# Optimization experiments

Measured on AMD Instinct MI355X. Metric: run time of the kernel, lower is better.

The kernel has to match this reference:

```python
import jax, jax.numpy as jnp
import numpy as np

REG_M = 0.1     # reg_m_bregman
N_ITER = 30     # fixed MM iteration count (POT uses numItermax=1000 w/ early stop)
EPS = 1e-16     # POT's stabilizer added to the denominator


def setup_inputs() -> dict:
    key = jax.random.key(0)
    kx, ky = jax.random.split(key)
    x = jax.random.normal(kx, (4096, 256), dtype=jnp.float32)
    y = jax.random.normal(ky, (4096, 256), dtype=jnp.float32)
    # L2-normalize embeddings so squared distances lie in [0,4] and the
    # KL kernel exp(-M / (2*reg_m)) stays in a representable range.
    x = x / jnp.linalg.norm(x, axis=1, keepdims=True)
    y = y / jnp.linalg.norm(y, axis=1, keepdims=True)
    return {"x": x, "y": y}


def reference(x, y):
    m, n = x.shape[0], y.shape[0]
    # ot.dist default metric: squared euclidean  M[i,j] = ||x_i - y_j||^2
    M = (jnp.sum(x * x, axis=1)[:, None]
         + jnp.sum(y * y, axis=1)[None, :]
         - 2.0 * (x @ y.T))                                  # [m, n]
    a = jnp.full((m,), 1.0 / m, dtype=x.dtype)
    b = jnp.full((n,), 1.0 / n, dtype=x.dtype)
    # POT mm_unbalanced, div='kl', reg_m1=reg_m2=reg_m, reg=0:
    # r1 = r2 = 1/2, K = sqrt(a_i b_j) * exp(-M / (2*reg_m)), G0 = a (x) b,
    # G <- K * G / (sqrt(rowsum_i) * sqrt(colsum_j) + eps)
    K = jnp.sqrt(a[:, None] * b[None, :]) * jnp.exp(-M / (2.0 * REG_M))
    G0 = a[:, None] * b[None, :]

    def step(G, _):
        Gd = jnp.sqrt(G.sum(axis=1)[:, None] * G.sum(axis=0)[None, :]) + EPS
        return K * G / Gd, None

    Pi, _ = jax.lax.scan(step, G0, None, length=N_ITER)
    # (Pi @ M.T).mean() = sum_j (sum_i Pi[i,j]) * (sum_k M[k,j]) / m^2
    return jnp.dot(Pi.sum(axis=0), M.sum(axis=0)) / (m * m)
```

## Files before the change

### kernel.cpp

```cpp
#include <hip/hip_runtime.h>
#include <math.h>

#define MDIM 4096
#define NDIM 4096
#define DDIM 256
#define N_ITER 30

#define TWO_KAPPA 14.426950408889634
#define CLCONST  (-12.0 - TWO_KAPPA)

typedef __attribute__((ext_vector_type(8))) short bf16x8;
typedef __attribute__((ext_vector_type(4))) float f32x4;

__device__ __forceinline__ unsigned encf(float f) {
  unsigned u = __float_as_uint(f);
  return (u & 0x80000000u) ? ~u : (u | 0x80000000u);
}
__device__ __forceinline__ float decf(unsigned u) {
  return __uint_as_float((u & 0x80000000u) ? (u ^ 0x80000000u) : ~u);
}

#define AL_RLX(p)      __hip_atomic_load((p), __ATOMIC_RELAXED, __HIP_MEMORY_SCOPE_AGENT)
#define AS_RLX(p, v)   __hip_atomic_store((p), (v), __ATOMIC_RELAXED, __HIP_MEMORY_SCOPE_AGENT)
#define AADD_RLX(p, v) __hip_atomic_fetch_add((p), (v), __ATOMIC_RELAXED, __HIP_MEMORY_SCOPE_AGENT)
#define AMAX_RLX(p, v) __hip_atomic_fetch_max((p), (v), __ATOMIC_RELAXED, __HIP_MEMORY_SCOPE_AGENT)

__global__ void norms_kernel(const float* __restrict__ x, const float* __restrict__ y,
                             float* __restrict__ xx, float* __restrict__ yy,
                             float* __restrict__ Sxx) {
  int wid = threadIdx.x >> 6, lane = threadIdx.x & 63;
  int row = blockIdx.x * 4 + wid;
  const float* src = (row < MDIM) ? x : y;
  int r = (row < MDIM) ? row : row - MDIM;
  const float4* p = (const float4*)(src + (size_t)r * DDIM);
  float4 v = p[lane];
  float s = v.x*v.x + v.y*v.y + v.z*v.z + v.w*v.w;
  #pragma unroll
  for (int off = 32; off; off >>= 1) s += __shfl_down(s, off);
  if (lane == 0) {
    if (row < MDIM) { xx[r] = s; atomicAdd(Sxx, s); }
    else            { yy[r] = s; }
  }
}

__global__ void sx_kernel(const float* __restrict__ x, float* __restrict__ sx) {
  int tx = threadIdx.x;
  int r0 = blockIdx.x * 16;
  float s = 0.f;
  #pragma unroll
  for (int r = 0; r < 16; ++r) s += x[(size_t)(r0 + r) * DDIM + tx];
  atomicAdd(&sx[tx], s);
}

__global__ void colM_kernel(const float* __restrict__ y, const float* __restrict__ sx,
                            const float* __restrict__ yy, const float* __restrict__ Sxx,
                            float* __restrict__ colM) {
  int wid = threadIdx.x >> 6, lane = threadIdx.x & 63;
  int j = blockIdx.x * 4 + wid;
  const float4* py = (const float4*)(y + (size_t)j * DDIM);
  const float4* ps = (const float4*)sx;
  float4 a = py[lane], b = ps[lane];
  float s = a.x*b.x + a.y*b.y + a.z*b.z + a.w*b.w;
  #pragma unroll
  for (int off = 32; off; off >>= 1) s += __shfl_down(s, off);
  if (lane == 0) colM[j] = *Sxx + (float)MDIM * yy[j] - 2.f * s;
}

__global__ void split_kernel(const float* __restrict__ x, const float* __restrict__ y,
                             ushort* __restrict__ xh, ushort* __restrict__ xl,
                             ushort* __restrict__ yh, ushort* __restrict__ yl) {
  int g = blockIdx.x * 256 + threadIdx.x;
  int e; const float4* src; ushort* dh; ushort* dl;
  if (g < 262144) { e = g;          src = (const float4*)x; dh = xh; dl = xl; }
  else            { e = g - 262144; src = (const float4*)y; dh = yh; dl = yl; }
  float4 v = src[e];
  float f[4] = {v.x, v.y, v.z, v.w};
  ushort hs[4], ls[4];
  #pragma unroll
  for (int i = 0; i < 4; ++i) {
    unsigned u = __float_as_uint(f[i]);
    unsigned hr = (u + 0x7FFFu + ((u >> 16) & 1u)) >> 16;
    hs[i] = (ushort)hr;
    float hf = __uint_as_float(hr << 16);
    float lo = f[i] - hf;
    unsigned ul = __float_as_uint(lo);
    unsigned lr = (ul + 0x7FFFu + ((ul >> 16) & 1u)) >> 16;
    ls[i] = (ushort)lr;
  }
  *(ushort4*)(dh + (size_t)e * 4) = make_ushort4(hs[0], hs[1], hs[2], hs[3]);
  *(ushort4*)(dl + (size_t)e * 4) = make_ushort4(ls[0], ls[1], ls[2], ls[3]);
}

#define GPAD 56
__global__ __launch_bounds__(256)
void gemm_mfma_kernel(const ushort* __restrict__ xh, const ushort* __restrict__ xl,
                      const ushort* __restrict__ yh, const ushort* __restrict__ yl,
                      short* __restrict__ D16, float* __restrict__ maxdot) {
  __shared__ ushort As[2][128][GPAD];
  __shared__ ushort Bs[2][128][GPAD];
  int tid = threadIdx.x;
  int lane = tid & 63, wid = tid >> 6;
  int bm = blockIdx.x & 31, bn = blockIdx.x >> 5;
  int wrow = (wid >> 1) * 64, wcol = (wid & 1) * 64;
  f32x4 acc[4][4] = {};

  int c0 = tid, c1 = tid + 256;
  int r0 = c0 >> 2, k80 = (c0 & 3) * 8;
  int r1 = c1 >> 2, k81 = (c1 & 3) * 8;
  const size_t arow0 = (size_t)(bm * 128 + r0) * DDIM;
  const size_t arow1 = (size_t)(bm * 128 + r1) * DDIM;
  const size_t brow0 = (size_t)(bn * 128 + r0) * DDIM;
  const size_t brow1 = (size_t)(bn * 128 + r1) * DDIM;

  for (int k0 = 0; k0 < DDIM; k0 += 32) {
    *(uint4*)&As[0][r0][k80] = *(const uint4*)(xh + arow0 + k0 + k80);
    *(uint4*)&As[0][r1][k81] = *(const uint4*)(xh + arow1 + k0 + k81);
    *(uint4*)&As[1][r0][k80] = *(const uint4*)(xl + arow0 + k0 + k80);
    *(uint4*)&As[1][r1][k81] = *(const uint4*)(xl + arow1 + k0 + k81);
    *(uint4*)&Bs[0][r0][k80] = *(const uint4*)(yh + brow0 + k0 + k80);
    *(uint4*)&Bs[0][r1][k81] = *(const uint4*)(yh + brow1 + k0 + k81);
    *(uint4*)&Bs[1][r0][k80] = *(const uint4*)(yl + brow0 + k0 + k80);
    *(uint4*)&Bs[1][r1][k81] = *(const uint4*)(yl + brow1 + k0 + k81);
    __syncthreads();
    int fr = lane & 15, kg = lane >> 4;
    bf16x8 ah[4], al[4], bh[4], bl[4];
    #pragma unroll
    for (int i = 0; i < 4; ++i) {
      ah[i] = *(const bf16x8*)&As[0][wrow + i * 16 + fr][kg * 8];
      al[i] = *(const bf16x8*)&As[1][wrow + i * 16 + fr][kg * 8];
      bh[i] = *(const bf16x8*)&Bs[0][wcol + i * 16 + fr][kg * 8];
      bl[i] = *(const bf16x8*)&Bs[1][wcol + i * 16 + fr][kg * 8];
    }
    #pragma unroll
    for (int i = 0; i < 4; ++i)
      #pragma unroll
      for (int j = 0; j < 4; ++j) {
        acc[i][j] = __builtin_amdgcn_mfma_f32_16x16x32_bf16(ah[i], bh[j], acc[i][j], 0, 0, 0);
        acc[i][j] = __builtin_amdgcn_mfma_f32_16x16x32_bf16(ah[i], bl[j], acc[i][j], 0, 0, 0);
        acc[i][j] = __builtin_amdgcn_mfma_f32_16x16x32_bf16(al[i], bh[j], acc[i][j], 0, 0, 0);
      }
    __syncthreads();
  }
  float tmax = -1.f;
  #pragma unroll
  for (int i = 0; i < 4; ++i) {
    #pragma unroll
    for (int j = 0; j < 4; ++j) {
      int col = bn * 128 + wcol + j * 16 + (lane & 15);
      #pragma unroll
      for (int r = 0; r < 4; ++r) {
        float d = acc[i][j][r];
        tmax = fmaxf(tmax, d);
        int q = __float2int_rn(fminf(fmaxf(d * 65536.f, -32767.f), 32767.f));
        int row = bm * 128 + wrow + i * 16 + (lane >> 4) * 4 + r;
        D16[(size_t)row * NDIM + col] = (short)q;
      }
    }
  }
  __shared__ float sm[4];
  #pragma unroll
  for (int off = 32; off; off >>= 1) tmax = fmaxf(tmax, __shfl_down(tmax, off));
  if (lane == 0) sm[wid] = tmax;
  __syncthreads();
  if (tid == 0) {
    float m = fmaxf(fmaxf(sm[0], sm[1]), fmaxf(sm[2], sm[3]));
    atomicMax((int*)maxdot, __float_as_int(fmaxf(m, 0.f)));
  }
}

__global__ __launch_bounds__(1024, 4)
void solve_kernel(const short* __restrict__ D16,
                  float* __restrict__ phi_pub, float* __restrict__ psi_pub,
                  const float* __restrict__ maxdot,
                  unsigned* rowMaxU, unsigned* colMaxU,
                  unsigned* rowFlag, unsigned* colFlag,
                  const float* __restrict__ colM,
                  float* lossacc, unsigned* lossdone,
                  float* __restrict__ out) {
  __shared__ float vec_lds[4096];
  __shared__ float red[32][33];
  __shared__ float own[32];
  __shared__ float sMax;
  int tid = threadIdx.x;
  int blk = blockIdx.x;
  bool rowside = blk < 128;
  int lloc = tid & 31;
  int chunk = tid >> 5;
  int obase = (rowside ? blk : (blk - 128)) * 32;
  float md = maxdot[0];

  unsigned* partnerFlag = rowside ? colFlag : rowFlag;
  unsigned* partnerMaxU = rowside ? colMaxU : rowMaxU;
  unsigned* myFlag      = rowside ? rowFlag : colFlag;
  unsigned* myMaxU      = rowside ? rowMaxU : colMaxU;
  const float* partnerPub = rowside ? psi_pub : phi_pub;
  float*       myPub      = rowside ? phi_pub : psi_pub;

  int2 d[32];
  if (rowside) {
    const short* src = D16 + (size_t)(obase + lloc) * NDIM + chunk * 128;
    #pragma unroll
    for (int g = 0; g < 32; ++g) d[g] = *(const int2*)(src + 4 * g);
  } else {
    int j = obase + lloc;
    #pragma unroll
    for (int g = 0; g < 32; ++g) {
      int rr = chunk * 128 + 4 * g;
      unsigned s0 = (unsigned short)(unsigned)D16[(size_t)(rr + 0) * NDIM + j];
      unsigned s1 = (unsigned short)(unsigned)D16[(size_t)(rr + 1) * NDIM + j];
      unsigned s2 = (unsigned short)(unsigned)D16[(size_t)(rr + 2) * NDIM + j];
      unsigned s3 = (unsigned short)(unsigned)D16[(size_t)(rr + 3) * NDIM + j];
      d[g].x = (int)(s0 | (s1 << 16));
      d[g].y = (int)(s2 | (s3 << 16));
    }
  }
  if (tid < 32) own[tid] = -6.f;

  int tEnd = rowside ? (N_ITER - 1) : N_ITER;
  for (int t = 1; t <= tEnd; ++t) {
    float sD  = (float)((double)t * (TWO_KAPPA / 65536.0));
    float tCL = (float)((double)t * CLCONST);
    float s2k = (float)((double)t * TWO_KAPPA);
    float tLmax = fmaf(s2k, md, tCL);

    float partnerMax;
    if (t == 1) partnerMax = -6.f;
    else {
      if (tid == 0) {
        while (AL_RLX(partnerFlag + t * 16) < 128u)
          __builtin_amdgcn_s_sleep(2);
        sMax = decf(AL_RLX(partnerMaxU + t * 16));
      }
      __syncthreads();
      partnerMax = sMax;
    }
    float Sh  = tLmax + partnerMax - 100.f;
    float Wsh = tCL - Sh;

    {
      float4 v;
      if (t == 1) {
        float c = -6.f + Wsh;
        v = make_float4(c, c, c, c);
      } else {
        const float* src = partnerPub + (size_t)(t & 1) * 4096 + tid * 4;
        unsigned long long a = AL_RLX((const unsigned long long*)src);
        unsigned long long b = AL_RLX((const unsigned long long*)(src + 2));
        v.x = __uint_as_float((unsigned)a) + Wsh;
        v.y = __uint_as_float((unsigned)(a >> 32)) + Wsh;
        v.z = __uint_as_float((unsigned)b) + Wsh;
        v.w = __uint_as_float((unsigned)(b >> 32)) + Wsh;
      }
      *(float4*)&vec_lds[tid * 4] = v;
    }
    __syncthreads();

    float a0 = 0.f, a1 = 0.f, a2 = 0.f, a3 = 0.f;
    #pragma unroll
    for (int g = 0; g < 32; ++g) {
      float4 pv = *(const float4*)&vec_lds[chunk * 128 + 4 * g];
      int2 dv = d[g];
      float d0 = (float)((short)(dv.x & 0xFFFF));
      float d1 = (float)(dv.x >> 16);
      float d2 = (float)((short)(dv.y & 0xFFFF));
      float d3 = (float)(dv.y >> 16);
      a0 += exp2f(fmaf(d0, sD, pv.x));
      a1 += exp2f(fmaf(d1, sD, pv.y));
      a2 += exp2f(fmaf(d2, sD, pv.z));
      a3 += exp2f(fmaf(d3, sD, pv.w));
    }
    red[lloc][chunk] = (a0 + a1) + (a2 + a3);
    __syncthreads();

    if (tid < 32) {
      float tot = 0.f;
      #pragma unroll
      for (int c = 0; c < 32; ++c) tot += red[tid][c];
      if (rowside || t < N_ITER) {
        float pn = 0.5f * (own[tid] - Sh - log2f(fmaxf(tot, 1e-30f)));
        own[tid] = pn;
        AS_RLX(myPub + (size_t)((t + 1) & 1) * 4096 + obase + tid, pn);
        float mx = pn;
        #pragma unroll
        for (int o = 16; o; o >>= 1) mx = fmaxf(mx, __shfl_down(mx, o));
        if (tid == 0) {
          AMAX_RLX(myMaxU + (t + 1) * 16, encf(mx));
          asm volatile("s_waitcnt vmcnt(0)" ::: "memory");
          AADD_RLX(myFlag + (t + 1) * 16, 1u);
        }
      } else {
        float contrib = exp2f(log2f(fmaxf(tot, 1e-30f)) + own[tid] + Sh
                              + log2f(colM[obase + tid]));
        #pragma unroll
        for (int o = 16; o; o >>= 1) contrib += __shfl_down(contrib, o);
        if (tid == 0) {
          AADD_RLX(&lossacc[blk & 15], contrib);
          asm volatile("s_waitcnt vmcnt(0)" ::: "memory");
          AADD_RLX(lossdone, 1u);
          if (blk == 128) {
            while (AL_RLX(lossdone) < 128u) __builtin_amdgcn_s_sleep(2);
            float tot2 = 0.f;
            #pragma unroll
            for (int s = 0; s < 16; ++s) tot2 += AL_RLX(&lossacc[s]);
            out[0] = tot2 * (1.f / ((float)MDIM * (float)MDIM));
          }
        }
      }
    }
  }
}

extern "C" void kernel_launch(void* const* d_in, const int* in_sizes, int n_in,
                              void* d_out, int out_size, void* d_ws, size_t ws_size,
                              hipStream_t stream) {
  const float* x = (const float*)d_in[0];
  const float* y = (const float*)d_in[1];
  float* out = (float*)d_out;

  char* ws = (char*)d_ws;
  size_t off = 0;
  auto alloc = [&](size_t bytes) -> void* {
    void* p = ws + off;
    off += (bytes + 255) & ~(size_t)255;
    return p;
  };
  short*    D16     = (short*)alloc((size_t)MDIM * NDIM * 2);
  ushort*   xh      = (ushort*)alloc((size_t)MDIM * DDIM * 2);
  ushort*   xl      = (ushort*)alloc((size_t)MDIM * DDIM * 2);
  ushort*   yh      = (ushort*)alloc((size_t)NDIM * DDIM * 2);
  ushort*   yl      = (ushort*)alloc((size_t)NDIM * DDIM * 2);
  float*    xx      = (float*)alloc(MDIM * 4);
  float*    yy      = (float*)alloc(NDIM * 4);
  float*    sx      = (float*)alloc(DDIM * 4);
  float*    colM    = (float*)alloc(NDIM * 4);
  float*    Sxx     = (float*)alloc(4);
  float*    maxd    = (float*)alloc(4);
  float*    phi_pub = (float*)alloc(2 * MDIM * 4);
  float*    psi_pub = (float*)alloc(2 * NDIM * 4);
  unsigned* rowMaxU = (unsigned*)alloc(32 * 16 * 4);
  unsigned* colMaxU = (unsigned*)alloc(32 * 16 * 4);
  unsigned* rowFlag = (unsigned*)alloc(32 * 16 * 4);
  unsigned* colFlag = (unsigned*)alloc(32 * 16 * 4);
  float*    lossacc = (float*)alloc(16 * 4);
  unsigned* lossdone= (unsigned*)alloc(16 * 4);

  hipMemsetAsync(Sxx, 0, 4, stream);
  hipMemsetAsync(maxd, 0, 4, stream);
  hipMemsetAsync(sx, 0, DDIM * 4, stream);
  hipMemsetAsync(rowMaxU, 0, 32 * 16 * 4, stream);
  hipMemsetAsync(colMaxU, 0, 32 * 16 * 4, stream);
  hipMemsetAsync(rowFlag, 0, 32 * 16 * 4, stream);
  hipMemsetAsync(colFlag, 0, 32 * 16 * 4, stream);
  hipMemsetAsync(lossacc, 0, 16 * 4, stream);
  hipMemsetAsync(lossdone, 0, 16 * 4, stream);

  norms_kernel<<<2048, 256, 0, stream>>>(x, y, xx, yy, Sxx);
  sx_kernel<<<256, 256, 0, stream>>>(x, sx);
  colM_kernel<<<1024, 256, 0, stream>>>(y, sx, yy, Sxx, colM);
  split_kernel<<<2048, 256, 0, stream>>>(x, y, xh, xl, yh, yl);
  gemm_mfma_kernel<<<1024, 256, 0, stream>>>(xh, xl, yh, yl, D16, maxd);

  void* kargs[] = {(void*)&D16, (void*)&phi_pub, (void*)&psi_pub,
                   (void*)&maxd, (void*)&rowMaxU, (void*)&colMaxU,
                   (void*)&rowFlag, (void*)&colFlag,
                   (void*)&colM, (void*)&lossacc, (void*)&lossdone,
                   (void*)&out};
  hipLaunchCooperativeKernel((void*)solve_kernel, dim3(256), dim3(1024),
                             kargs, 0, stream);
}
```

Measured before the change: 1.027 ms.

## Restructure solver so each block owns a 16-row stripe in LDS and computes both sums

Replaces the row-side/column-side block split with 256 blocks that each hold a 16-row stripe of the quantized distance matrix in shared memory. Every iteration, each block computes row sums for its own rows and per-block column partial sums in a single pass of exp evaluations. The column partials are published to a global buffer and reduced across blocks after a grid-wide flag barrier. This removes the duplicated exp work and the strided transposed load of the column side. In exchange it adds a second grid barrier per iteration and a 4 MB partial-sum buffer that is written and read every iteration.

```diff
diff --git a/kernel.cpp b/kernel.cpp
--- a/kernel.cpp
+++ b/kernel.cpp
@@ -168,141 +168,172 @@
   }
 }
 
-__global__ __launch_bounds__(1024, 4)
+__global__ __launch_bounds__(1024)
 void solve_kernel(const short* __restrict__ D16,
-                  float* __restrict__ phi_pub, float* __restrict__ psi_pub,
+                  float* __restrict__ colp,
+                  float* __restrict__ psi_pub,
                   const float* __restrict__ maxdot,
-                  unsigned* rowMaxU, unsigned* colMaxU,
-                  unsigned* rowFlag, unsigned* colFlag,
+                  unsigned* phimaxS, unsigned* psimaxS,
+                  unsigned* flag1, unsigned* flag2,
                   const float* __restrict__ colM,
                   float* lossacc, unsigned* lossdone,
                   float* __restrict__ out) {
-  __shared__ float vec_lds[4096];
-  __shared__ float red[32][33];
-  __shared__ float own[32];
-  __shared__ float sMax;
-  int tid = threadIdx.x;
-  int blk = blockIdx.x;
-  bool rowside = blk < 128;
-  int lloc = tid & 31;
-  int chunk = tid >> 5;
-  int obase = (rowside ? blk : (blk - 128)) * 32;
+  __shared__ ushort stripeS[16 * 4096];
+  __shared__ float  vecS[4096];
+  __shared__ float  redrow[16][16];
+  __shared__ float  red2[16][16];
+  __shared__ float  ownS[16];
+  __shared__ float  sS[2];
+  int tid = threadIdx.x, lane = tid & 63, wid = tid >> 6;
+  int b = blockIdx.x;
   float md = maxdot[0];
 
-  unsigned* partnerFlag = rowside ? colFlag : rowFlag;
-  unsigned* partnerMaxU = rowside ? colMaxU : rowMaxU;
-  unsigned* myFlag      = rowside ? rowFlag : colFlag;
-  unsigned* myMaxU      = rowside ? rowMaxU : colMaxU;
-  const float* partnerPub = rowside ? psi_pub : phi_pub;
-  float*       myPub      = rowside ? phi_pub : psi_pub;
-
-  int2 d[32];
-  if (rowside) {
-    const short* src = D16 + (size_t)(obase + lloc) * NDIM + chunk * 128;
+  {
+    const uint4* src = (const uint4*)(D16 + (size_t)b * 16 * NDIM);
+    uint4* dst = (uint4*)stripeS;
     #pragma unroll
-    for (int g = 0; g < 32; ++g) d[g] = *(const int2*)(src + 4 * g);
-  } else {
-    int j = obase + lloc;
-    #pragma unroll
-    for (int g = 0; g < 32; ++g) {
-      int rr = chunk * 128 + 4 * g;
-      unsigned s0 = (unsigned short)(unsigned)D16[(size_t)(rr + 0) * NDIM + j];
-      unsigned s1 = (unsigned short)(unsigned)D16[(size_t)(rr + 1) * NDIM + j];
-      unsigned s2 = (unsigned short)(unsigned)D16[(size_t)(rr + 2) * NDIM + j];
-      unsigned s3 = (unsigned short)(unsigned)D16[(size_t)(rr + 3) * NDIM + j];
-      d[g].x = (int)(s0 | (s1 << 16));
-      d[g].y = (int)(s2 | (s3 << 16));
-    }
-  }
-  if (tid < 32) own[tid] = -6.f;
-
-  int tEnd = rowside ? (N_ITER - 1) : N_ITER;
-  for (int t = 1; t <= tEnd; ++t) {
+    for (int k = 0; k < 8; ++k) dst[tid + 1024 * k] = src[tid + 1024 * k];
+  }
+  if (tid < 16) ownS[tid] = -6.f;
+  __syncthreads();
+
+  for (int t = 1; t <= N_ITER; ++t) {
     float sD  = (float)((double)t * (TWO_KAPPA / 65536.0));
     float tCL = (float)((double)t * CLCONST);
     float s2k = (float)((double)t * TWO_KAPPA);
+
+    if (t > 1) {
+      if (tid == 0) {
+        while (AL_RLX(&flag2[(t - 1) * 16]) < 256u) __builtin_amdgcn_s_sleep(2);
+        unsigned uf = 0, up = 0;
+        #pragma unroll
+        for (int s = 0; s < 16; ++s) {
+          unsigned a = AL_RLX(&phimaxS[t * 16 + s]); uf = a > uf ? a : uf;
+          unsigned c = AL_RLX(&psimaxS[t * 16 + s]); up = c > up ? c : up;
+        }
+        sS[0] = decf(uf); sS[1] = decf(up);
+      }
+      __syncthreads();
+    }
+    float fm = (t == 1) ? -6.f : sS[0];
+    float pm = (t == 1) ? -6.f : sS[1];
     float tLmax = fmaf(s2k, md, tCL);
-
-    float partnerMax;
-    if (t == 1) partnerMax = -6.f;
-    else {
-      if (tid == 0) {
-        while (AL_RLX(partnerFlag + t * 16) < 128u)
-          __builtin_amdgcn_s_sleep(2);
-        sMax = decf(AL_RLX(partnerMaxU + t * 16));
-      }
-      __syncthreads();
-      partnerMax = sMax;
-    }
-    float Sh  = tLmax + partnerMax - 100.f;
-    float Wsh = tCL - Sh;
-
-    {
+    float S  = tLmax + fm + pm - 100.f;
+    float WS = tCL - S;
+
+    if (t == 1) {
+      *(float4*)&vecS[4 * tid] = make_float4(-6.f, -6.f, -6.f, -6.f);
+    } else {
+      const unsigned long long* sp =
+          (const unsigned long long*)(psi_pub + (size_t)(t & 1) * 4096 + 4 * tid);
+      unsigned long long a = AL_RLX(sp), c = AL_RLX(sp + 1);
       float4 v;
-      if (t == 1) {
-        float c = -6.f + Wsh;
-        v = make_float4(c, c, c, c);
-      } else {
-        const float* src = partnerPub + (size_t)(t & 1) * 4096 + tid * 4;
-        unsigned long long a = AL_RLX((const unsigned long long*)src);
-        unsigned long long b = AL_RLX((const unsigned long long*)(src + 2));
-        v.x = __uint_as_float((unsigned)a) + Wsh;
-        v.y = __uint_as_float((unsigned)(a >> 32)) + Wsh;
-        v.z = __uint_as_float((unsigned)b) + Wsh;
-        v.w = __uint_as_float((unsigned)(b >> 32)) + Wsh;
-      }
-      *(float4*)&vec_lds[tid * 4] = v;
-    }
-    __syncthreads();
-
-    float a0 = 0.f, a1 = 0.f, a2 = 0.f, a3 = 0.f;
+      v.x = __uint_as_float((unsigned)a); v.y = __uint_as_float((unsigned)(a >> 32));
+      v.z = __uint_as_float((unsigned)c); v.w = __uint_as_float((unsigned)(c >> 32));
+      *(float4*)&vecS[4 * tid] = v;
+    }
+    __syncthreads();
+
+    float4 psi4 = *(const float4*)&vecS[4 * tid];
+    float P0 = psi4.x + WS, P1 = psi4.y + WS, P2 = psi4.z + WS, P3 = psi4.w + WS;
+    float c0 = 0.f, c1 = 0.f, c2 = 0.f, c3 = 0.f;
+    float rs[16];
     #pragma unroll
-    for (int g = 0; g < 32; ++g) {
-      float4 pv = *(const float4*)&vec_lds[chunk * 128 + 4 * g];
-      int2 dv = d[g];
+    for (int r = 0; r < 16; ++r) {
+      float phr = ownS[r];
+      int2 dv = *(const int2*)(stripeS + r * 4096 + 4 * tid);
       float d0 = (float)((short)(dv.x & 0xFFFF));
       float d1 = (float)(dv.x >> 16);
       float d2 = (float)((short)(dv.y & 0xFFFF));
       float d3 = (float)(dv.y >> 16);
-      a0 += exp2f(fmaf(d0, sD, pv.x));
-      a1 += exp2f(fmaf(d1, sD, pv.y));
-      a2 += exp2f(fmaf(d2, sD, pv.z));
-      a3 += exp2f(fmaf(d3, sD, pv.w));
-    }
-    red[lloc][chunk] = (a0 + a1) + (a2 + a3);
-    __syncthreads();
-
-    if (tid < 32) {
+      float e0 = exp2f(fmaf(d0, sD, P0 + phr));
+      float e1 = exp2f(fmaf(d1, sD, P1 + phr));
+      float e2 = exp2f(fmaf(d2, sD, P2 + phr));
+      float e3 = exp2f(fmaf(d3, sD, P3 + phr));
+      c0 += e0; c1 += e1; c2 += e2; c3 += e3;
+      rs[r] = (e0 + e1) + (e2 + e3);
+    }
+    {
+      unsigned long long u0 = ((unsigned long long)__float_as_uint(c1) << 32) | __float_as_uint(c0);
+      unsigned long long u1 = ((unsigned long long)__float_as_uint(c3) << 32) | __float_as_uint(c2);
+      unsigned long long* cp = (unsigned long long*)(colp + (size_t)b * 4096 + 4 * tid);
+      AS_RLX(cp, u0); AS_RLX(cp + 1, u1);
+    }
+    if (t < N_ITER) {
+      #pragma unroll
+      for (int r = 0; r < 16; ++r) {
+        float v = rs[r];
+        #pragma unroll
+        for (int o = 32; o; o >>= 1) v += __shfl_down(v, o);
+        if (lane == 0) redrow[r][wid] = v;
+      }
+      __syncthreads();
+      if (tid < 16) {
+        float s = 0.f;
+        #pragma unroll
+        for (int w = 0; w < 16; ++w) s += redrow[tid][w];
+        float pn = ownS[tid] - 0.5f * (S + log2f(fmaxf(s, 1e-30f)));
+        ownS[tid] = pn;
+        float mx = pn;
+        #pragma unroll
+        for (int o = 8; o; o >>= 1) mx = fmaxf(mx, __shfl_down(mx, o));
+        if (tid == 0) AMAX_RLX(&phimaxS[(t + 1) * 16 + (b & 15)], encf(mx));
+      }
+    }
+    asm volatile("s_waitcnt vmcnt(0)" ::: "memory");
+    __syncthreads();
+    if (tid == 0) {
+      AADD_RLX(&flag1[t * 16], 1u);
+      while (AL_RLX(&flag1[t * 16]) < 256u) __builtin_amdgcn_s_sleep(2);
+    }
+    __syncthreads();
+
+    {
+      int k  = tid >> 2;
+      int cq = (tid & 3) * 4;
+      const unsigned long long* rp =
+          (const unsigned long long*)(colp + (size_t)k * 4096 + 16 * b + cq);
+      unsigned long long a = AL_RLX(rp), c = AL_RLX(rp + 1);
+      float f0 = __uint_as_float((unsigned)a), f1 = __uint_as_float((unsigned)(a >> 32));
+      float f2 = __uint_as_float((unsigned)c), f3 = __uint_as_float((unsigned)(c >> 32));
+      #pragma unroll
+      for (int o = 4; o < 64; o <<= 1) {
+        f0 += __shfl_down(f0, o); f1 += __shfl_down(f1, o);
+        f2 += __shfl_down(f2, o); f3 += __shfl_down(f3, o);
+      }
+      if (lane < 4) *(float4*)&red2[wid][lane * 4] = make_float4(f0, f1, f2, f3);
+    }
+    __syncthreads();
+    if (tid < 16) {
       float tot = 0.f;
       #pragma unroll
-      for (int c = 0; c < 32; ++c) tot += red[tid][c];
-      if (rowside || t < N_ITER) {
-        float pn = 0.5f * (own[tid] - Sh - log2f(fmaxf(tot, 1e-30f)));
-        own[tid] = pn;
-        AS_RLX(myPub + (size_t)((t + 1) & 1) * 4096 + obase + tid, pn);
+      for (int w = 0; w < 16; ++w) tot += red2[w][tid];
+      int jj = 16 * b + tid;
+      if (t < N_ITER) {
+        float pn = vecS[jj] - 0.5f * (S + log2f(fmaxf(tot, 1e-30f)));
+        AS_RLX(&psi_pub[(size_t)((t + 1) & 1) * 4096 + jj], pn);
         float mx = pn;
         #pragma unroll
-        for (int o = 16; o; o >>= 1) mx = fmaxf(mx, __shfl_down(mx, o));
+        for (int o = 8; o; o >>= 1) mx = fmaxf(mx, __shfl_down(mx, o));
         if (tid == 0) {
-          AMAX_RLX(myMaxU + (t + 1) * 16, encf(mx));
+          AMAX_RLX(&psimaxS[(t + 1) * 16 + (b & 15)], encf(mx));
           asm volatile("s_waitcnt vmcnt(0)" ::: "memory");
-          AADD_RLX(myFlag + (t + 1) * 16, 1u);
+          AADD_RLX(&flag2[t * 16], 1u);
         }
       } else {
-        float contrib = exp2f(log2f(fmaxf(tot, 1e-30f)) + own[tid] + Sh
-                              + log2f(colM[obase + tid]));
-        #pragma unroll
-        for (int o = 16; o; o >>= 1) contrib += __shfl_down(contrib, o);
+        float term = (tot * 9.094947017729282e-13f) * colM[jj];
+        #pragma unroll
+        for (int o = 8; o; o >>= 1) term += __shfl_down(term, o);
         if (tid == 0) {
-          AADD_RLX(&lossacc[blk & 15], contrib);
+          AADD_RLX(&lossacc[b & 15], term);
           asm volatile("s_waitcnt vmcnt(0)" ::: "memory");
           AADD_RLX(lossdone, 1u);
-          if (blk == 128) {
-            while (AL_RLX(lossdone) < 128u) __builtin_amdgcn_s_sleep(2);
-            float tot2 = 0.f;
+          if (b == 0) {
+            while (AL_RLX(lossdone) < 256u) __builtin_amdgcn_s_sleep(2);
+            float tt = 0.f;
             #pragma unroll
-            for (int s = 0; s < 16; ++s) tot2 += AL_RLX(&lossacc[s]);
-            out[0] = tot2 * (1.f / ((float)MDIM * (float)MDIM));
+            for (int s = 0; s < 16; ++s) tt += AL_RLX(&lossacc[s]);
+            out[0] = exp2f(log2f(tt) + S + 16.f);
           }
         }
       }
@@ -325,6 +356,7 @@
     return p;
   };
   short*    D16     = (short*)alloc((size_t)MDIM * NDIM * 2);
+  float*    colp    = (float*)alloc((size_t)256 * NDIM * 4);
   ushort*   xh      = (ushort*)alloc((size_t)MDIM * DDIM * 2);
   ushort*   xl      = (ushort*)alloc((size_t)MDIM * DDIM * 2);
   ushort*   yh      = (ushort*)alloc((size_t)NDIM * DDIM * 2);
@@ -335,22 +367,21 @@
   float*    colM    = (float*)alloc(NDIM * 4);
   float*    Sxx     = (float*)alloc(4);
   float*    maxd    = (float*)alloc(4);
-  float*    phi_pub = (float*)alloc(2 * MDIM * 4);
   float*    psi_pub = (float*)alloc(2 * NDIM * 4);
-  unsigned* rowMaxU = (unsigned*)alloc(32 * 16 * 4);
-  unsigned* colMaxU = (unsigned*)alloc(32 * 16 * 4);
-  unsigned* rowFlag = (unsigned*)alloc(32 * 16 * 4);
-  unsigned* colFlag = (unsigned*)alloc(32 * 16 * 4);
+  unsigned* phimaxS = (unsigned*)alloc(32 * 16 * 4);
+  unsigned* psimaxS = (unsigned*)alloc(32 * 16 * 4);
+  unsigned* flag1   = (unsigned*)alloc(32 * 16 * 4);
+  unsigned* flag2   = (unsigned*)alloc(32 * 16 * 4);
   float*    lossacc = (float*)alloc(16 * 4);
   unsigned* lossdone= (unsigned*)alloc(16 * 4);
 
   hipMemsetAsync(Sxx, 0, 4, stream);
   hipMemsetAsync(maxd, 0, 4, stream);
   hipMemsetAsync(sx, 0, DDIM * 4, stream);
-  hipMemsetAsync(rowMaxU, 0, 32 * 16 * 4, stream);
-  hipMemsetAsync(colMaxU, 0, 32 * 16 * 4, stream);
-  hipMemsetAsync(rowFlag, 0, 32 * 16 * 4, stream);
-  hipMemsetAsync(colFlag, 0, 32 * 16 * 4, stream);
+  hipMemsetAsync(phimaxS, 0, 32 * 16 * 4, stream);
+  hipMemsetAsync(psimaxS, 0, 32 * 16 * 4, stream);
+  hipMemsetAsync(flag1, 0, 32 * 16 * 4, stream);
+  hipMemsetAsync(flag2, 0, 32 * 16 * 4, stream);
   hipMemsetAsync(lossacc, 0, 16 * 4, stream);
   hipMemsetAsync(lossdone, 0, 16 * 4, stream);
 
@@ -360,9 +391,9 @@
   split_kernel<<<2048, 256, 0, stream>>>(x, y, xh, xl, yh, yl);
   gemm_mfma_kernel<<<1024, 256, 0, stream>>>(xh, xl, yh, yl, D16, maxd);
 
-  void* kargs[] = {(void*)&D16, (void*)&phi_pub, (void*)&psi_pub,
-                   (void*)&maxd, (void*)&rowMaxU, (void*)&colMaxU,
-                   (void*)&rowFlag, (void*)&colFlag,
+  void* kargs[] = {(void*)&D16, (void*)&colp, (void*)&psi_pub,
+                   (void*)&maxd, (void*)&phimaxS, (void*)&psimaxS,
+                   (void*)&flag1, (void*)&flag2,
                    (void*)&colM, (void*)&lossacc, (void*)&lossdone,
                    (void*)&out};
   hipLaunchCooperativeKernel((void*)solve_kernel, dim3(256), dim3(1024),
```

Result: faster. 989.4 us (-3.6%).
